# Kernel tuning notes

Hardware: AMD Instinct MI355X
Metric: run time of the kernel (lower is better)

## Reference

```python
import jax, jax.numpy as jnp
import numpy as np

B_, N_, E_, NNZ = 64, 1723, 1723, 16384
CIN, COUT = 256, 256
H1, H2, H3 = 64, 32, 128  # lin1 out, HGCN hidden, HGCN out (hidden_channels=128)


def layernorm(x, g, b, eps=1e-5):
    mu = jnp.mean(x, axis=-1, keepdims=True)
    var = jnp.mean((x - mu) ** 2, axis=-1, keepdims=True)
    return (x - mu) * jax.lax.rsqrt(var + eps) * g + b


def graph_linear(x, W, b):
    # x: (B, Cin, N) -> (B, Cout, N), matches torch.matmul(W[None], x) + b[None,:,None]
    return jnp.einsum('oc,bcn->bon', W, x) + b[None, :, None]


def hconv(x, node_idx, edge_idx, theta, bias):
    # PyG HypergraphConv (no attention): X' = D^-1 H W B^-1 H^T X Theta + bias
    x = jnp.einsum('bnc,oc->bno', x, theta)  # lin (bias=False)
    ones = jnp.ones(node_idx.shape, x.dtype)
    Dd = jax.ops.segment_sum(ones, node_idx, num_segments=N_)  # node degree
    Bd = jax.ops.segment_sum(ones, edge_idx, num_segments=E_)  # hyperedge degree
    Dinv = jnp.where(Dd > 0, 1.0 / Dd, 0.0)
    Binv = jnp.where(Bd > 0, 1.0 / Bd, 0.0)
    # node -> hyperedge aggregation, message scaled by B^-1 of target edge
    msg = jnp.swapaxes(x[:, node_idx, :] * Binv[edge_idx][None, :, None], 0, 1)  # (nnz,B,C)
    ef = jax.ops.segment_sum(msg, edge_idx, num_segments=E_)  # (E,B,C)
    # hyperedge -> node aggregation, message scaled by D^-1 of target node
    msg2 = ef[edge_idx] * Dinv[node_idx][:, None, None]  # (nnz,B,C)
    out = jax.ops.segment_sum(msg2, node_idx, num_segments=N_)  # (N,B,C)
    return jnp.swapaxes(out, 0, 1) + bias


def setup_inputs():
    key = jax.random.key(0)
    ks = jax.random.split(key, 8)
    s = 0.02
    return {
        'x': jax.random.normal(ks[0], (B_, N_, CIN), jnp.float32),
        'incident_matrix': jax.random.randint(ks[1], (2, NNZ), 0, N_, jnp.int32),
        'pre_g': jnp.ones((CIN,), jnp.float32),
        'pre_b': jnp.zeros((CIN,), jnp.float32),
        'lin1_W': jax.random.normal(ks[2], (H1, CIN), jnp.float32) * s,
        'lin1_b': jnp.zeros((H1,), jnp.float32),
        'n1_g': jnp.ones((H1,), jnp.float32),
        'n1_b': jnp.zeros((H1,), jnp.float32),
        'th1': jax.random.normal(ks[3], (H2, H1), jnp.float32) * s,
        'bi1': jnp.zeros((H2,), jnp.float32),
        'th2': jax.random.normal(ks[4], (H3, H2), jnp.float32) * s,
        'bi2': jnp.zeros((H3,), jnp.float32),
        'n2_g': jnp.ones((H3,), jnp.float32),
        'n2_b': jnp.zeros((H3,), jnp.float32),
        'lin2_W': jax.random.normal(ks[5], (COUT, H3), jnp.float32) * s,
        'lin2_b': jnp.zeros((COUT,), jnp.float32),
    }


def reference(x, incident_matrix, pre_g, pre_b, lin1_W, lin1_b, n1_g, n1_b,
              th1, bi1, th2, bi2, n2_g, n2_b, lin2_W, lin2_b):
    node_idx, edge_idx = incident_matrix[0], incident_matrix[1]
    ty = jnp.swapaxes(jax.nn.relu(layernorm(x, pre_g, pre_b)), 1, 2)  # (B,Cin,N)
    y = jnp.swapaxes(graph_linear(ty, lin1_W, lin1_b), 1, 2)          # (B,N,64)
    y = jax.nn.relu(layernorm(y, n1_g, n1_b))
    y = hconv(y, node_idx, edge_idx, th1, bi1)                         # (B,N,32)
    y = hconv(y, node_idx, edge_idx, th2, bi2)                         # (B,N,128)
    ty = jnp.swapaxes(jax.nn.relu(layernorm(y, n2_g, n2_b)), 1, 2)
    y = jnp.swapaxes(graph_linear(ty, lin2_W, lin2_b), 1, 2)           # (B,N,256)
    return x + y  # skip_conv declared in module but unused in forward
```

## Files before the change

### kernel.cpp

```cpp
#include <hip/hip_runtime.h>
#include <cstdint>

constexpr int B  = 64;
constexpr int N  = 1723;
constexpr int E  = 1723;
constexpr int NNZ = 16384;
constexpr int ROWS = B * N;

typedef __bf16 bf16x8 __attribute__((ext_vector_type(8)));
typedef float  f32x4  __attribute__((ext_vector_type(4)));

constexpr size_t OFF_DD   = 0;
constexpr size_t OFF_BD   = OFF_DD + E;
constexpr size_t OFF_NCUR = OFF_BD + E;
constexpr size_t OFF_ECUR = OFF_NCUR + E;
constexpr size_t OFF_NOFF = OFF_ECUR + E;
constexpr size_t OFF_EOFF = OFF_NOFF + (E + 1);
constexpr size_t OFF_NVAL = OFF_EOFF + (E + 1);
constexpr size_t OFF_EVAL = OFF_NVAL + NNZ;

constexpr int WB_LIN1 = 0;
constexpr int WB_TH1  = 16384;
constexpr int WB_TH2  = 18432;
constexpr int WB_LIN2 = 22528;
constexpr int WB_TOT  = 55296;
constexpr int CVT_BLOCKS  = WB_TOT / 8 / 256;
constexpr int ZERO_INTS   = 4 * E;
constexpr int ZERO_BLOCKS = (ZERO_INTS + 255) / 256;

constexpr size_t B_WB    = 262144;
constexpr size_t B_SLOTA = 1u << 20;
constexpr size_t B_SLOTB = B_SLOTA + (30u << 20);
constexpr size_t B_SLOTC = B_SLOTB + (8u << 20);
constexpr size_t B_SLOTD = B_SLOTC + (8u << 20);

__device__ __forceinline__ ushort f2bf(float f) {
  uint32_t b = __float_as_uint(f);
  b += 0x7fffu + ((b >> 16) & 1u);
  return (ushort)(b >> 16);
}
__device__ __forceinline__ float bf2f(ushort u) {
  return __uint_as_float((uint32_t)u << 16);
}
union U16x8 { uint4 q; ushort s[8]; };

__global__ __launch_bounds__(256) void k_init(const float* __restrict__ W1, const float* __restrict__ W2,
                                              const float* __restrict__ W3, const float* __restrict__ W4,
                                              ushort* __restrict__ out, int* __restrict__ zr) {
  int bid = blockIdx.x;
  if (bid < CVT_BLOCKS) {
    int e = (bid * 256 + threadIdx.x) * 8;
    const float* src;
    int off;
    if (e < WB_TH1)      { src = W1; off = e - WB_LIN1; }
    else if (e < WB_TH2) { src = W2; off = e - WB_TH1; }
    else if (e < WB_LIN2){ src = W3; off = e - WB_TH2; }
    else                 { src = W4; off = e - WB_LIN2; }
    float4 v0 = *(const float4*)(src + off);
    float4 v1 = *(const float4*)(src + off + 4);
    U16x8 u;
    u.s[0] = f2bf(v0.x); u.s[1] = f2bf(v0.y); u.s[2] = f2bf(v0.z); u.s[3] = f2bf(v0.w);
    u.s[4] = f2bf(v1.x); u.s[5] = f2bf(v1.y); u.s[6] = f2bf(v1.z); u.s[7] = f2bf(v1.w);
    *(uint4*)(out + e) = u.q;
  } else {
    int i = (bid - CVT_BLOCKS) * 256 + threadIdx.x;
    if (i < ZERO_INTS) zr[i] = 0;
  }
}

__global__ __launch_bounds__(256) void k_hist(const int* __restrict__ inc,
                                              int* __restrict__ Dd, int* __restrict__ Bd) {
  int k = blockIdx.x * 256 + threadIdx.x;
  atomicAdd(&Dd[inc[k]], 1);
  atomicAdd(&Bd[inc[NNZ + k]], 1);
}

__global__ __launch_bounds__(256) void k_scan(const int* __restrict__ Dd, const int* __restrict__ Bd,
                                              int* __restrict__ noff, int* __restrict__ eoff) {
  __shared__ int part[256];
  const int t = threadIdx.x;
  for (int pass = 0; pass < 2; ++pass) {
    const int* cnt = pass ? Bd : Dd;
    int* off = pass ? eoff : noff;
    constexpr int CH = 7;
    int loc[CH];
    int s = 0;
    int base = t * CH;
#pragma unroll
    for (int i = 0; i < CH; ++i) {
      int idx = base + i;
      loc[i] = (idx < E) ? cnt[idx] : 0;
      s += loc[i];
    }
    part[t] = s;
    __syncthreads();
    for (int d = 1; d < 256; d <<= 1) {
      int v = (t >= d) ? part[t - d] : 0;
      __syncthreads();
      part[t] += v;
      __syncthreads();
    }
    int pre = (t > 0) ? part[t - 1] : 0;
#pragma unroll
    for (int i = 0; i < CH; ++i) {
      int idx = base + i;
      if (idx < E) off[idx] = pre;
      pre += loc[i];
    }
    if (t == 255) off[E] = pre;
    __syncthreads();
  }
}

__global__ __launch_bounds__(256) void k_fill(const int* __restrict__ inc,
                                              const int* __restrict__ noff, const int* __restrict__ eoff,
                                              int* __restrict__ ncur, int* __restrict__ ecur,
                                              int* __restrict__ nval, int* __restrict__ eval) {
  int k = blockIdx.x * 256 + threadIdx.x;
  int n = inc[k], e = inc[NNZ + k];
  int p = atomicAdd(&ecur[e], 1);
  eval[eoff[e] + p] = n;
  int q = atomicAdd(&ncur[n], 1);
  nval[noff[n] + q] = e;
}

__global__ __launch_bounds__(256) void k_sort2(const int* __restrict__ noff, int* __restrict__ nval,
                                               const int* __restrict__ eoff, int* __restrict__ eval) {
  int s = blockIdx.x * 256 + threadIdx.x;
  const int* off;
  int* vals;
  if (s < E) { off = noff; vals = nval; }
  else if (s < 2 * E) { off = eoff; vals = eval; s -= E; }
  else return;
  int b = off[s], e = off[s + 1];
  for (int i = b + 1; i < e; ++i) {
    int v = vals[i];
    int j = i - 1;
    while (j >= b && vals[j] > v) { vals[j + 1] = vals[j]; --j; }
    vals[j + 1] = v;
  }
}

__global__ __launch_bounds__(256, 2) void k_lin1th1(const float* __restrict__ x,
                                                    const ushort* __restrict__ Wb,
                                                    const float* __restrict__ lin1_b,
                                                    const float* __restrict__ pre_g,
                                                    const float* __restrict__ pre_b,
                                                    const float* __restrict__ n1_g,
                                                    const float* __restrict__ n1_b,
                                                    ushort* __restrict__ xl1) {
  __shared__ __align__(16) uint4 R0[2048];
  __shared__ __align__(16) uint4 R1[2048];
  __shared__ __align__(16) uint4 W2s[256];
  __shared__ float2 st[64];

  const int t = threadIdx.x;
  const int r0 = blockIdx.x * 64;
  const ushort* W1 = Wb + WB_LIN1;
  const ushort* W2 = Wb + WB_TH1;

  {
    int row = t >> 3, c = t & 7;
    W2s[row * 8 + (c ^ (row & 7))] = *(const uint4*)(W2 + row * 64 + c * 8);
  }
#pragma unroll
  for (int i = 0; i < 8; ++i) {
    int idx = t + i * 256;
    int row = idx >> 5, c = idx & 31;
    R1[row * 32 + (c ^ (row & 7))] = *(const uint4*)(W1 + row * 256 + c * 8);
  }
#pragma unroll
  for (int i = 0; i < 8; ++i) {
    int idx = t + i * 256;
    int row = idx >> 5, c = idx & 31;
    const float* src = x + (size_t)(r0 + row) * 256 + c * 8;
    float4 v0 = *(const float4*)src;
    float4 v1 = *(const float4*)(src + 4);
    U16x8 u;
    u.s[0] = f2bf(v0.x); u.s[1] = f2bf(v0.y); u.s[2] = f2bf(v0.z); u.s[3] = f2bf(v0.w);
    u.s[4] = f2bf(v1.x); u.s[5] = f2bf(v1.y); u.s[6] = f2bf(v1.z); u.s[7] = f2bf(v1.w);
    R0[row * 32 + (c ^ (row & 7))] = u.q;
  }
  __syncthreads();

  {
    int row = t >> 2, part = t & 3;
    float s1 = 0.f, s2 = 0.f;
#pragma unroll
    for (int i = 0; i < 8; ++i) {
      int c = part * 8 + i;
      U16x8 u; u.q = R0[row * 32 + (c ^ (row & 7))];
#pragma unroll
      for (int j = 0; j < 8; ++j) { float v = bf2f(u.s[j]); s1 += v; s2 += v * v; }
    }
    s1 += __shfl_xor(s1, 1, 64); s2 += __shfl_xor(s2, 1, 64);
    s1 += __shfl_xor(s1, 2, 64); s2 += __shfl_xor(s2, 2, 64);
    if (part == 0) {
      float mu = s1 / 256.f;
      float var = fmaxf(s2 / 256.f - mu * mu, 0.f);
      st[row] = make_float2(mu, rsqrtf(var + 1e-5f));
    }
  }
  __syncthreads();
#pragma unroll
  for (int i = 0; i < 8; ++i) {
    int idx = t + i * 256;
    int row = idx >> 5, c = idx & 31;
    int slot = row * 32 + (c ^ (row & 7));
    U16x8 u; u.q = R0[slot];
    float2 s = st[row];
    float4 g0 = *(const float4*)(pre_g + c * 8);
    float4 g1 = *(const float4*)(pre_g + c * 8 + 4);
    float4 b0 = *(const float4*)(pre_b + c * 8);
    float4 b1 = *(const float4*)(pre_b + c * 8 + 4);
    U16x8 o;
    o.s[0] = f2bf(fmaxf(fmaf((bf2f(u.s[0]) - s.x) * s.y, g0.x, b0.x), 0.f));
    o.s[1] = f2bf(fmaxf(fmaf((bf2f(u.s[1]) - s.x) * s.y, g0.y, b0.y), 0.f));
    o.s[2] = f2bf(fmaxf(fmaf((bf2f(u.s[2]) - s.x) * s.y, g0.z, b0.z), 0.f));
    o.s[3] = f2bf(fmaxf(fmaf((bf2f(u.s[3]) - s.x) * s.y, g0.w, b0.w), 0.f));
    o.s[4] = f2bf(fmaxf(fmaf((bf2f(u.s[4]) - s.x) * s.y, g1.x, b1.x), 0.f));
    o.s[5] = f2bf(fmaxf(fmaf((bf2f(u.s[5]) - s.x) * s.y, g1.y, b1.y), 0.f));
    o.s[6] = f2bf(fmaxf(fmaf((bf2f(u.s[6]) - s.x) * s.y, g1.z, b1.z), 0.f));
    o.s[7] = f2bf(fmaxf(fmaf((bf2f(u.s[7]) - s.x) * s.y, g1.w, b1.w), 0.f));
    R0[slot] = o.q;
  }
  __syncthreads();

  const int lane = t & 63;
  const int w = t >> 6;
  const int lo = lane & 15, hi = lane >> 4;
  const int wm = w & 1, wn = w >> 1;
  const int m0 = wm * 32 + lo, m1 = wm * 32 + 16 + lo;
  const bf16x8* Asv = (const bf16x8*)R0;
  const bf16x8* Wsv = (const bf16x8*)R1;
  f32x4 acc1[2][2] = {};
#pragma unroll
  for (int ks = 0; ks < 8; ++ks) {
    int cb = ks * 4 + hi;
    bf16x8 a0 = Asv[m0 * 32 + (cb ^ (m0 & 7))];
    bf16x8 a1 = Asv[m1 * 32 + (cb ^ (m1 & 7))];
#pragma unroll
    for (int f = 0; f < 2; ++f) {
      int n = wn * 32 + f * 16 + lo;
      bf16x8 bfr = Wsv[n * 32 + (cb ^ (n & 7))];
      acc1[0][f] = __builtin_amdgcn_mfma_f32_16x16x32_bf16(a0, bfr, acc1[0][f], 0, 0, 0);
      acc1[1][f] = __builtin_amdgcn_mfma_f32_16x16x32_bf16(a1, bfr, acc1[1][f], 0, 0, 0);
    }
  }
  __syncthreads();

  float* ost = (float*)R1;
#pragma unroll
  for (int f = 0; f < 2; ++f) {
    int colg = wn * 32 + f * 16 + lo;
    float badd = lin1_b[colg];
#pragma unroll
    for (int i = 0; i < 2; ++i)
#pragma unroll
      for (int r = 0; r < 4; ++r) {
        int lr = wm * 32 + i * 16 + hi * 4 + r;
        ost[lr * 68 + colg] = acc1[i][f][r] + badd;
      }
  }
  __syncthreads();

  {
    int row = t >> 2, part = t & 3;
    float s1 = 0.f, s2 = 0.f;
#pragma unroll
    for (int i = 0; i < 16; ++i) {
      float v = ost[row * 68 + part * 16 + i];
      s1 += v; s2 += v * v;
    }
    s1 += __shfl_xor(s1, 1, 64); s2 += __shfl_xor(s2, 1, 64);
    s1 += __shfl_xor(s1, 2, 64); s2 += __shfl_xor(s2, 2, 64);
    if (part == 0) {
      float mu = s1 / 64.f;
      float var = fmaxf(s2 / 64.f - mu * mu, 0.f);
      st[row] = make_float2(mu, rsqrtf(var + 1e-5f));
    }
  }
  __syncthreads();
#pragma unroll
  for (int i = 0; i < 2; ++i) {
    int idx = t + i * 256;
    int row = idx >> 3, c = idx & 7;
    float2 s = st[row];
    U16x8 u;
#pragma unroll
    for (int j = 0; j < 8; ++j) {
      int col = c * 8 + j;
      float v = ost[row * 68 + col];
      u.s[j] = f2bf(fmaxf(fmaf((v - s.x) * s.y, n1_g[col], n1_b[col]), 0.f));
    }
    R0[row * 8 + (c ^ (row & 7))] = u.q;
  }
  __syncthreads();

  f32x4 acc2[2] = {};
#pragma unroll
  for (int ks = 0; ks < 2; ++ks) {
    int cb = ks * 4 + hi;
    bf16x8 a0 = Asv[m0 * 8 + (cb ^ (m0 & 7))];
    bf16x8 a1 = Asv[m1 * 8 + (cb ^ (m1 & 7))];
    int n = wn * 16 + lo;
    bf16x8 bfr = ((const bf16x8*)W2s)[n * 8 + (cb ^ (n & 7))];
    acc2[0] = __builtin_amdgcn_mfma_f32_16x16x32_bf16(a0, bfr, acc2[0], 0, 0, 0);
    acc2[1] = __builtin_amdgcn_mfma_f32_16x16x32_bf16(a1, bfr, acc2[1], 0, 0, 0);
  }
  __syncthreads();
  {
    int colg = wn * 16 + lo;
#pragma unroll
    for (int i = 0; i < 2; ++i)
#pragma unroll
      for (int r = 0; r < 4; ++r) {
        int lr = wm * 32 + i * 16 + hi * 4 + r;
        ost[lr * 36 + colg] = acc2[i][r];
      }
  }
  __syncthreads();
  {
    int lr = t >> 2, c8 = t & 3;
    uint32_t r = r0 + lr;
    uint32_t b_ = r / (uint32_t)N;
    uint32_t n_ = r - b_ * (uint32_t)N;
    U16x8 u;
#pragma unroll
    for (int j = 0; j < 8; ++j) u.s[j] = f2bf(ost[lr * 36 + c8 * 8 + j]);
    *(uint4*)(xl1 + ((size_t)n_ * 64 + b_) * 32 + c8 * 8) = u.q;
  }
}

template <bool HASB>
__global__ __launch_bounds__(256) void agg_bf16_k(const ushort* __restrict__ in,
                                                  const int* __restrict__ off,
                                                  const int* __restrict__ vals,
                                                  const float* __restrict__ bias,
                                                  ushort* __restrict__ outb) {
  const int seg = blockIdx.x;
  const int beg = off[seg], end = off[seg + 1];
  const int t = threadIdx.x;
  float acc[8] = {0.f, 0.f, 0.f, 0.f, 0.f, 0.f, 0.f, 0.f};
  for (int k = beg; k < end; ++k) {
    int src = vals[k];
    U16x8 u;
    u.q = *(const uint4*)(in + (size_t)src * 2048 + t * 8);
#pragma unroll
    for (int j = 0; j < 8; ++j) acc[j] += bf2f(u.s[j]);
  }
  float inv = (end > beg) ? 1.f / (float)(end - beg) : 0.f;
  U16x8 o;
  if constexpr (HASB) {
    int cb = (t & 3) * 8;
#pragma unroll
    for (int j = 0; j < 8; ++j) o.s[j] = f2bf(acc[j] * inv + bias[cb + j]);
  } else {
#pragma unroll
    for (int j = 0; j < 8; ++j) o.s[j] = f2bf(acc[j] * inv);
  }
  *(uint4*)(outb + (size_t)seg * 2048 + t * 8) = o.q;
}

__global__ __launch_bounds__(256, 2) void k_aggth2(const ushort* __restrict__ ef2,
                                                   const int* __restrict__ noff,
                                                   const int* __restrict__ nval,
                                                   const ushort* __restrict__ W2b,
                                                   const float* __restrict__ bi2,
                                                   const float* __restrict__ n2_g,
                                                   const float* __restrict__ n2_b,
                                                   ushort* __restrict__ y3n) {
  __shared__ __align__(16) uint4 A2s[256];
  __shared__ __align__(16) uint4 W2s[512];
  __shared__ float ost[64 * 132];
  __shared__ float2 st[64];
  const int t = threadIdx.x;
  const int seg = blockIdx.x;

#pragma unroll
  for (int i = 0; i < 2; ++i) {
    int idx = t + i * 256;
    int row = idx >> 2, c = idx & 3;
    W2s[row * 4 + (c ^ (row & 3))] = *(const uint4*)(W2b + row * 32 + c * 8);
  }
  const int beg = noff[seg], end = noff[seg + 1];
  float acc[8] = {0.f, 0.f, 0.f, 0.f, 0.f, 0.f, 0.f, 0.f};
  for (int k = beg; k < end; ++k) {
    int src = nval[k];
    U16x8 u;
    u.q = *(const uint4*)(ef2 + (size_t)src * 2048 + t * 8);
#pragma unroll
    for (int j = 0; j < 8; ++j) acc[j] += bf2f(u.s[j]);
  }
  float inv = (end > beg) ? 1.f / (float)(end - beg) : 0.f;
  {
    U16x8 u;
#pragma unroll
    for (int j = 0; j < 8; ++j) u.s[j] = f2bf(acc[j] * inv);
    int row = t >> 2, c = t & 3;
    A2s[row * 4 + (c ^ (row & 3))] = u.q;
  }
  __syncthreads();

  const int lane = t & 63;
  const int w = t >> 6;
  const int lo = lane & 15, hi = lane >> 4;
  const int wm = w & 1, wn = w >> 1;
  const int m0 = wm * 32 + lo, m1 = wm * 32 + 16 + lo;
  const bf16x8* Asv = (const bf16x8*)A2s;
  const bf16x8* Wsv = (const bf16x8*)W2s;
  f32x4 acc2[2][4] = {};
  {
    bf16x8 a0 = Asv[m0 * 4 + (hi ^ (m0 & 3))];
    bf16x8 a1 = Asv[m1 * 4 + (hi ^ (m1 & 3))];
#pragma unroll
    for (int f = 0; f < 4; ++f) {
      int n = wn * 64 + f * 16 + lo;
      bf16x8 bfr = Wsv[n * 4 + (hi ^ (n & 3))];
      acc2[0][f] = __builtin_amdgcn_mfma_f32_16x16x32_bf16(a0, bfr, acc2[0][f], 0, 0, 0);
      acc2[1][f] = __builtin_amdgcn_mfma_f32_16x16x32_bf16(a1, bfr, acc2[1][f], 0, 0, 0);
    }
  }
#pragma unroll
  for (int f = 0; f < 4; ++f) {
    int colg = wn * 64 + f * 16 + lo;
    float badd = bi2[colg];
#pragma unroll
    for (int i = 0; i < 2; ++i)
#pragma unroll
      for (int r = 0; r < 4; ++r) {
        int lr = wm * 32 + i * 16 + hi * 4 + r;
        ost[lr * 132 + colg] = acc2[i][f][r] + badd;
      }
  }
  __syncthreads();
  {
    int row = t >> 2, part = t & 3;
    float s1 = 0.f, s2 = 0.f;
#pragma unroll
    for (int i = 0; i < 32; ++i) {
      float v = ost[row * 132 + part * 32 + i];
      s1 += v; s2 += v * v;
    }
    s1 += __shfl_xor(s1, 1, 64); s2 += __shfl_xor(s2, 1, 64);
    s1 += __shfl_xor(s1, 2, 64); s2 += __shfl_xor(s2, 2, 64);
    if (part == 0) {
      float mu = s1 / 128.f;
      float var = fmaxf(s2 / 128.f - mu * mu, 0.f);
      st[row] = make_float2(mu, rsqrtf(var + 1e-5f));
    }
  }
  __syncthreads();
#pragma unroll
  for (int i = 0; i < 4; ++i) {
    int idx = t + i * 256;
    int row = idx >> 4, c = idx & 15;
    float2 s = st[row];
    U16x8 u;
#pragma unroll
    for (int j = 0; j < 8; ++j) {
      int col = c * 8 + j;
      float v = ost[row * 132 + col];
      u.s[j] = f2bf(fmaxf(fmaf((v - s.x) * s.y, n2_g[col], n2_b[col]), 0.f));
    }
    *(uint4*)(y3n + ((size_t)seg * 64 + row) * 128 + c * 8) = u.q;
  }
}

__global__ __launch_bounds__(256, 2) void k_lin2(const ushort* __restrict__ y3n,
                                                 const ushort* __restrict__ Wl2,
                                                 const float* __restrict__ lin2_b,
                                                 const float* __restrict__ x,
                                                 float* __restrict__ out) {
  __shared__ __align__(16) uint4 smem[2048];
  const int t = threadIdx.x;
  const int bid = blockIdx.x;
  const int tile = bid & 3;
  const int r0 = (bid >> 2) * 64;
  const int c0 = tile * 64;
  uint4* AsQ = smem;
  uint4* WsQ = smem + 1024;

#pragma unroll
  for (int i = 0; i < 4; ++i) {
    int idx = t + i * 256;
    int row = idx >> 4, c = idx & 15;
    AsQ[row * 16 + (c ^ (row & 7))] = *(const uint4*)(y3n + (size_t)(r0 + row) * 128 + c * 8);
  }
#pragma unroll
  for (int i = 0; i < 4; ++i) {
    int idx = t + i * 256;
    int row = idx >> 4, c = idx & 15;
    WsQ[row * 16 + (c ^ (row & 7))] = *(const uint4*)(Wl2 + (size_t)(c0 + row) * 128 + c * 8);
  }
  __syncthreads();

  const int lane = t & 63;
  const int w = t >> 6;
  const int lo = lane & 15, hi = lane >> 4;
  const int wm = w & 1, wn = w >> 1;
  const int m0 = wm * 32 + lo, m1 = wm * 32 + 16 + lo;
  const bf16x8* Asv = (const bf16x8*)AsQ;
  const bf16x8* Wsv = (const bf16x8*)WsQ;
  f32x4 acc[2][2] = {};
#pragma unroll
  for (int ks = 0; ks < 4; ++ks) {
    int cb = ks * 4 + hi;
    bf16x8 a0 = Asv[m0 * 16 + (cb ^ (m0 & 7))];
    bf16x8 a1 = Asv[m1 * 16 + (cb ^ (m1 & 7))];
#pragma unroll
    for (int f = 0; f < 2; ++f) {
      int n = wn * 32 + f * 16 + lo;
      bf16x8 bfr = Wsv[n * 16 + (cb ^ (n & 7))];
      acc[0][f] = __builtin_amdgcn_mfma_f32_16x16x32_bf16(a0, bfr, acc[0][f], 0, 0, 0);
      acc[1][f] = __builtin_amdgcn_mfma_f32_16x16x32_bf16(a1, bfr, acc[1][f], 0, 0, 0);
    }
  }
  __syncthreads();

  float* ost = (float*)smem;
#pragma unroll
  for (int f = 0; f < 2; ++f) {
    int cl = wn * 32 + f * 16 + lo;
    float badd = lin2_b[c0 + cl];
#pragma unroll
    for (int i = 0; i < 2; ++i)
#pragma unroll
      for (int r = 0; r < 4; ++r) {
        int lr = wm * 32 + i * 16 + hi * 4 + r;
        ost[lr * 68 + cl] = acc[i][f][r] + badd;
      }
  }
  __syncthreads();

#pragma unroll
  for (int i = 0; i < 4; ++i) {
    int idx = t + i * 256;
    int lr = idx >> 4, c4 = idx & 15;
    uint32_t r = r0 + lr;
    uint32_t n_ = r >> 6, b_ = r & 63u;
    size_t obase = ((size_t)b_ * N + n_) * 256 + c0 + c4 * 4;
    float4 v = *(const float4*)&ost[lr * 68 + c4 * 4];
    float4 s = *(const float4*)(x + obase);
    v.x += s.x; v.y += s.y; v.z += s.z; v.w += s.w;
    *(float4*)(out + obase) = v;
  }
}

extern "C" void kernel_launch(void* const* d_in, const int* in_sizes, int n_in,
                              void* d_out, int out_size, void* d_ws, size_t ws_size,
                              hipStream_t stream) {
  const float* x      = (const float*)d_in[0];
  const int*   inc    = (const int*)  d_in[1];
  const float* pre_g  = (const float*)d_in[2];
  const float* pre_b  = (const float*)d_in[3];
  const float* lin1_W = (const float*)d_in[4];
  const float* lin1_b = (const float*)d_in[5];
  const float* n1_g   = (const float*)d_in[6];
  const float* n1_b   = (const float*)d_in[7];
  const float* th1    = (const float*)d_in[8];
  const float* bi1    = (const float*)d_in[9];
  const float* th2    = (const float*)d_in[10];
  const float* bi2    = (const float*)d_in[11];
  const float* n2_g   = (const float*)d_in[12];
  const float* n2_b   = (const float*)d_in[13];
  const float* lin2_W = (const float*)d_in[14];
  const float* lin2_b = (const float*)d_in[15];
  float* out = (float*)d_out;
  char* ws = (char*)d_ws;

  int* meta = (int*)ws;
  int* Dd   = meta + OFF_DD;
  int* Bd   = meta + OFF_BD;
  int* ncur = meta + OFF_NCUR;
  int* ecur = meta + OFF_ECUR;
  int* noff = meta + OFF_NOFF;
  int* eoff = meta + OFF_EOFF;
  int* nval = meta + OFF_NVAL;
  int* eval = meta + OFF_EVAL;

  ushort* Wbase = (ushort*)(ws + B_WB);
  ushort* y3n = (ushort*)(ws + B_SLOTA);
  ushort* xl1 = (ushort*)(ws + B_SLOTB);
  ushort* ef2 = (ushort*)(ws + B_SLOTB);
  ushort* ef1 = (ushort*)(ws + B_SLOTC);
  ushort* y2  = (ushort*)(ws + B_SLOTD);

  k_init<<<CVT_BLOCKS + ZERO_BLOCKS, 256, 0, stream>>>(lin1_W, th1, th2, lin2_W, Wbase, meta);

  k_hist<<<NNZ / 256, 256, 0, stream>>>(inc, Dd, Bd);
  k_scan<<<1, 256, 0, stream>>>(Dd, Bd, noff, eoff);
  k_fill<<<NNZ / 256, 256, 0, stream>>>(inc, noff, eoff, ncur, ecur, nval, eval);
  k_sort2<<<(2 * E + 255) / 256, 256, 0, stream>>>(noff, nval, eoff, eval);

  k_lin1th1<<<ROWS / 64, 256, 0, stream>>>(x, Wbase, lin1_b, pre_g, pre_b, n1_g, n1_b, xl1);

  agg_bf16_k<false><<<E, 256, 0, stream>>>(xl1, eoff, eval, nullptr, ef1);
  agg_bf16_k<true ><<<E, 256, 0, stream>>>(ef1, noff, nval, bi1, y2);
  agg_bf16_k<false><<<E, 256, 0, stream>>>(y2, eoff, eval, nullptr, ef2);

  k_aggth2<<<E, 256, 0, stream>>>(ef2, noff, nval, Wbase + WB_TH2, bi2, n2_g, n2_b, y3n);

  k_lin2<<<(ROWS / 64) * 4, 256, 0, stream>>>(y3n, Wbase + WB_LIN2, lin2_b, x, out);
}
```

Before: 191.7 us.

## Hold lin1 weights in registers, shrink LDS, and remap lin2 blocks per XCD

In the fused lin1/th1 kernel, each thread now loads its lin1 weight fragments straight from global memory into registers instead of staging them in a second LDS buffer. The output staging and the th1 input buffer reuse the single remaining LDS region, and one barrier is dropped. Together these cut LDS use so the launch bound can go from 2 to 3 blocks per SIMD. In k_lin2, block IDs are remapped so consecutive work tiles land on the same XCD, improving L2 locality for the shared row tiles. The costs are higher register pressure from 16 bf16x8 weight fragments per thread and redundant global weight loads across blocks.

```diff
diff --git a/kernel.cpp b/kernel.cpp
--- a/kernel.cpp
+++ b/kernel.cpp
@@ -141,7 +141,7 @@
   }
 }
 
-__global__ __launch_bounds__(256, 2) void k_lin1th1(const float* __restrict__ x,
+__global__ __launch_bounds__(256, 3) void k_lin1th1(const float* __restrict__ x,
                                                     const ushort* __restrict__ Wb,
                                                     const float* __restrict__ lin1_b,
                                                     const float* __restrict__ pre_g,
@@ -150,7 +150,6 @@
                                                     const float* __restrict__ n1_b,
                                                     ushort* __restrict__ xl1) {
   __shared__ __align__(16) uint4 R0[2048];
-  __shared__ __align__(16) uint4 R1[2048];
   __shared__ __align__(16) uint4 W2s[256];
   __shared__ float2 st[64];
 
@@ -159,15 +158,24 @@
   const ushort* W1 = Wb + WB_LIN1;
   const ushort* W2 = Wb + WB_TH1;
 
+  const int lane = t & 63;
+  const int w = t >> 6;
+  const int lo = lane & 15, hi = lane >> 4;
+  const int wm = w & 1, wn = w >> 1;
+  const int m0 = wm * 32 + lo, m1 = wm * 32 + 16 + lo;
+
+  bf16x8 wf[16];
+#pragma unroll
+  for (int ks = 0; ks < 8; ++ks)
+#pragma unroll
+    for (int f = 0; f < 2; ++f) {
+      int n = wn * 32 + f * 16 + lo;
+      wf[ks * 2 + f] = *(const bf16x8*)(W1 + (size_t)n * 256 + (ks * 4 + hi) * 8);
+    }
+
   {
     int row = t >> 3, c = t & 7;
     W2s[row * 8 + (c ^ (row & 7))] = *(const uint4*)(W2 + row * 64 + c * 8);
-  }
-#pragma unroll
-  for (int i = 0; i < 8; ++i) {
-    int idx = t + i * 256;
-    int row = idx >> 5, c = idx & 31;
-    R1[row * 32 + (c ^ (row & 7))] = *(const uint4*)(W1 + row * 256 + c * 8);
   }
 #pragma unroll
   for (int i = 0; i < 8; ++i) {
@@ -226,13 +234,7 @@
   }
   __syncthreads();
 
-  const int lane = t & 63;
-  const int w = t >> 6;
-  const int lo = lane & 15, hi = lane >> 4;
-  const int wm = w & 1, wn = w >> 1;
-  const int m0 = wm * 32 + lo, m1 = wm * 32 + 16 + lo;
   const bf16x8* Asv = (const bf16x8*)R0;
-  const bf16x8* Wsv = (const bf16x8*)R1;
   f32x4 acc1[2][2] = {};
 #pragma unroll
   for (int ks = 0; ks < 8; ++ks) {
@@ -241,15 +243,13 @@
     bf16x8 a1 = Asv[m1 * 32 + (cb ^ (m1 & 7))];
 #pragma unroll
     for (int f = 0; f < 2; ++f) {
-      int n = wn * 32 + f * 16 + lo;
-      bf16x8 bfr = Wsv[n * 32 + (cb ^ (n & 7))];
-      acc1[0][f] = __builtin_amdgcn_mfma_f32_16x16x32_bf16(a0, bfr, acc1[0][f], 0, 0, 0);
-      acc1[1][f] = __builtin_amdgcn_mfma_f32_16x16x32_bf16(a1, bfr, acc1[1][f], 0, 0, 0);
-    }
-  }
-  __syncthreads();
-
-  float* ost = (float*)R1;
+      acc1[0][f] = __builtin_amdgcn_mfma_f32_16x16x32_bf16(a0, wf[ks * 2 + f], acc1[0][f], 0, 0, 0);
+      acc1[1][f] = __builtin_amdgcn_mfma_f32_16x16x32_bf16(a1, wf[ks * 2 + f], acc1[1][f], 0, 0, 0);
+    }
+  }
+  __syncthreads();
+
+  float* ost = (float*)R0;
 #pragma unroll
   for (int f = 0; f < 2; ++f) {
     int colg = wn * 32 + f * 16 + lo;
@@ -281,6 +281,7 @@
     }
   }
   __syncthreads();
+  uint4* A2q = R0 + 1152;
 #pragma unroll
   for (int i = 0; i < 2; ++i) {
     int idx = t + i * 256;
@@ -293,22 +294,22 @@
       float v = ost[row * 68 + col];
       u.s[j] = f2bf(fmaxf(fmaf((v - s.x) * s.y, n1_g[col], n1_b[col]), 0.f));
     }
-    R0[row * 8 + (c ^ (row & 7))] = u.q;
-  }
-  __syncthreads();
-
+    A2q[row * 8 + (c ^ (row & 7))] = u.q;
+  }
+  __syncthreads();
+
+  const bf16x8* A2v = (const bf16x8*)A2q;
   f32x4 acc2[2] = {};
 #pragma unroll
   for (int ks = 0; ks < 2; ++ks) {
     int cb = ks * 4 + hi;
-    bf16x8 a0 = Asv[m0 * 8 + (cb ^ (m0 & 7))];
-    bf16x8 a1 = Asv[m1 * 8 + (cb ^ (m1 & 7))];
+    bf16x8 a0 = A2v[m0 * 8 + (cb ^ (m0 & 7))];
+    bf16x8 a1 = A2v[m1 * 8 + (cb ^ (m1 & 7))];
     int n = wn * 16 + lo;
     bf16x8 bfr = ((const bf16x8*)W2s)[n * 8 + (cb ^ (n & 7))];
     acc2[0] = __builtin_amdgcn_mfma_f32_16x16x32_bf16(a0, bfr, acc2[0], 0, 0, 0);
     acc2[1] = __builtin_amdgcn_mfma_f32_16x16x32_bf16(a1, bfr, acc2[1], 0, 0, 0);
   }
-  __syncthreads();
   {
     int colg = wn * 16 + lo;
 #pragma unroll
@@ -467,6 +468,7 @@
   }
 }
 
+constexpr int NWG2 = (ROWS / 64) * 4;
 __global__ __launch_bounds__(256, 2) void k_lin2(const ushort* __restrict__ y3n,
                                                  const ushort* __restrict__ Wl2,
                                                  const float* __restrict__ lin2_b,
@@ -474,9 +476,13 @@
                                                  float* __restrict__ out) {
   __shared__ __align__(16) uint4 smem[2048];
   const int t = threadIdx.x;
-  const int bid = blockIdx.x;
-  const int tile = bid & 3;
-  const int r0 = (bid >> 2) * 64;
+  int orig = blockIdx.x;
+  int xcd = orig & 7;
+  int idx0 = orig >> 3;
+  constexpr int q = NWG2 / 8, r = NWG2 % 8;
+  int wgid = (xcd < r ? xcd * (q + 1) : r * (q + 1) + (xcd - r) * q) + idx0;
+  const int tile = wgid & 3;
+  const int r0 = (wgid >> 2) * 64;
   const int c0 = tile * 64;
   uint4* AsQ = smem;
   uint4* WsQ = smem + 1024;
@@ -526,9 +532,9 @@
 #pragma unroll
     for (int i = 0; i < 2; ++i)
 #pragma unroll
-      for (int r = 0; r < 4; ++r) {
-        int lr = wm * 32 + i * 16 + hi * 4 + r;
-        ost[lr * 68 + cl] = acc[i][f][r] + badd;
+      for (int r2 = 0; r2 < 4; ++r2) {
+        int lr = wm * 32 + i * 16 + hi * 4 + r2;
+        ost[lr * 68 + cl] = acc[i][f][r2] + badd;
       }
   }
   __syncthreads();
@@ -537,8 +543,8 @@
   for (int i = 0; i < 4; ++i) {
     int idx = t + i * 256;
     int lr = idx >> 4, c4 = idx & 15;
-    uint32_t r = r0 + lr;
-    uint32_t n_ = r >> 6, b_ = r & 63u;
+    uint32_t rr = r0 + lr;
+    uint32_t n_ = rr >> 6, b_ = rr & 63u;
     size_t obase = ((size_t)b_ * N + n_) * 256 + c0 + c4 * 4;
     float4 v = *(const float4*)&ost[lr * 68 + c4 * 4];
     float4 s = *(const float4*)(x + obase);
@@ -601,5 +607,5 @@
 
   k_aggth2<<<E, 256, 0, stream>>>(ef2, noff, nval, Wbase + WB_TH2, bi2, n2_g, n2_b, y3n);
 
-  k_lin2<<<(ROWS / 64) * 4, 256, 0, stream>>>(y3n, Wbase + WB_LIN2, lin2_b, x, out);
-}
+  k_lin2<<<NWG2, 256, 0, stream>>>(y3n, Wbase + WB_LIN2, lin2_b, x, out);
+}
```

Measured after the change: 182.7 us. 1.05x faster.
